# Performance work log

Hardware: AMD Instinct MI355X
Metric: run time of the kernel (lower is better)

Reference implementation:

```python
import jax, jax.numpy as jnp
import numpy as np

N = 200000
F_IN = 165
H = 128
E = 3200000


def gcn_conv(x, edge_index, W, b):
    # x: [N, Fin], edge_index: [2, E], W: [Fin, Fout], b: [Fout]
    n = x.shape[0]
    h = x @ W  # linear transform first (PyG GCNConv)
    # add self loops
    loops = jnp.arange(n, dtype=edge_index.dtype)
    src = jnp.concatenate([edge_index[0], loops])
    dst = jnp.concatenate([edge_index[1], loops])
    # symmetric normalization: deg computed on dst (in-degree incl. self loops)
    deg = jax.ops.segment_sum(jnp.ones_like(dst, dtype=h.dtype), dst, num_segments=n)
    dinv = jnp.where(deg > 0, jax.lax.rsqrt(deg), 0.0)
    norm = dinv[src] * dinv[dst]  # [E+N]
    msgs = h[src] * norm[:, None]  # gather + scale
    out = jax.ops.segment_sum(msgs, dst, num_segments=n)  # scatter-add
    return out + b


def setup_inputs() -> dict:
    key = jax.random.key(0)
    k = jax.random.split(key, 8)
    x = jax.random.normal(k[0], (N, F_IN), dtype=jnp.float32)
    edge_index = jax.random.randint(k[1], (2, E), 0, N, dtype=jnp.int64)
    s1 = 1.0 / np.sqrt(F_IN)
    s2 = 1.0 / np.sqrt(H)
    W1 = jax.random.uniform(k[2], (F_IN, H), jnp.float32, -s1, s1)
    b1 = jnp.zeros((H,), jnp.float32)
    W2 = jax.random.uniform(k[3], (H, H), jnp.float32, -s2, s2)
    b2 = jnp.zeros((H,), jnp.float32)
    Wl = jax.random.uniform(k[4], (H, 2), jnp.float32, -s2, s2)
    bl = jax.random.uniform(k[5], (2,), jnp.float32, -s2, s2)
    return {"x": x, "edge_index": edge_index, "W1": W1, "b1": b1,
            "W2": W2, "b2": b2, "Wl": Wl, "bl": bl}


def reference(x, edge_index, W1, b1, W2, b2, Wl, bl):
    h = gcn_conv(x, edge_index, W1, b1)
    h = jax.nn.relu(h)
    # dropout p=0.3 is identity in eval mode
    h = gcn_conv(h, edge_index, W2, b2)
    h = jax.nn.relu(h)
    return h @ Wl + bl  # [N, 2]
```

## Files before the change

### kernel.cpp

```cpp
#include <hip/hip_runtime.h>
#include <hip/hip_bf16.h>

#define FIN 165
#define HID 128
#define NPB 256
#define MAXNB 784
#define CAP 4608
#define EPB 2048

typedef __attribute__((ext_vector_type(8))) short short8;
typedef __attribute__((ext_vector_type(4))) float float4v;

__device__ inline unsigned bf16rne(float v) {
    unsigned u = __float_as_uint(v);
    return (u + 0x7fffu + ((u >> 16) & 1u)) >> 16;
}

__device__ inline void bf16split(float v, short& h, short& l) {
    unsigned u = __float_as_uint(v);
    unsigned r = u + 0x7fffu + ((u >> 16) & 1u);
    h = (short)(r >> 16);
    float hf = __uint_as_float(((unsigned)(unsigned short)h) << 16);
    float lf = v - hf;
    unsigned u2 = __float_as_uint(lf);
    unsigned r2 = u2 + 0x7fffu + ((u2 >> 16) & 1u);
    l = (short)(r2 >> 16);
}

__global__ __launch_bounds__(256) void bucket_scatter(const int* __restrict__ src,
                                                      const int* __restrict__ dst,
                                                      int* __restrict__ gcur,
                                                      unsigned* __restrict__ bucketed,
                                                      int E, int n, int NB) {
    __shared__ int hist[MAXNB];
    __shared__ int base[MAXNB];
    __shared__ int lcur[MAXNB];
    int tid = threadIdx.x;
    long e0 = (long)blockIdx.x * EPB;
    for (int b = tid; b < NB; b += 256) { hist[b] = 0; lcur[b] = 0; }
    __syncthreads();
    int sv[EPB / 256], dv[EPB / 256];
#pragma unroll
    for (int i = 0; i < EPB / 256; ++i) {
        long e = e0 + i * 256 + tid;
        sv[i] = (e < E) ? src[e] : -1;
        dv[i] = (e < E) ? dst[e] : -1;
        if ((unsigned)dv[i] < (unsigned)n && (unsigned)sv[i] < (unsigned)n)
            atomicAdd(&hist[dv[i] >> 8], 1);
    }
    __syncthreads();
    for (int b = tid; b < NB; b += 256) {
        int h = hist[b];
        base[b] = h ? atomicAdd(&gcur[b * 16], h) : 0;
    }
    __syncthreads();
#pragma unroll
    for (int i = 0; i < EPB / 256; ++i) {
        int d = dv[i], s = sv[i];
        if ((unsigned)d < (unsigned)n && (unsigned)s < (unsigned)n) {
            int bk = d >> 8;
            int idx = base[bk] + atomicAdd(&lcur[bk], 1);
            if ((unsigned)idx < (unsigned)CAP)
                bucketed[(size_t)bk * CAP + idx] =
                    (unsigned)s | ((unsigned)(d & 255) << 18);
        }
    }
}

__global__ __launch_bounds__(256) void bucket_scan(const int* __restrict__ gcur,
                                                   int* __restrict__ bb, int NB,
                                                   int* __restrict__ rowptr, int n) {
    __shared__ int part[256];
    int t = threadIdx.x;
    int v[4];
    int s = 0;
#pragma unroll
    for (int i = 0; i < 4; ++i) {
        int b = t * 4 + i;
        v[i] = (b < NB) ? gcur[b * 16] : 0;
        s += v[i];
    }
    part[t] = s;
    __syncthreads();
    for (int off = 1; off < 256; off <<= 1) {
        int x = (t >= off) ? part[t - off] : 0;
        __syncthreads();
        part[t] += x;
        __syncthreads();
    }
    int run = part[t] - s;
#pragma unroll
    for (int i = 0; i < 4; ++i) {
        int b = t * 4 + i;
        if (b < NB) bb[b] = run;
        run += v[i];
    }
    if (t == 255) { bb[NB] = run; rowptr[n] = run; }
}

__global__ __launch_bounds__(256) void build_csr(const unsigned* __restrict__ bucketed,
                                                 const int* __restrict__ bb,
                                                 float* __restrict__ dinv,
                                                 int* __restrict__ rowptr,
                                                 int* __restrict__ col, int n) {
    __shared__ int deg[NPB];
    __shared__ int scn[NPB];
    __shared__ int cur[NPB];
    int b = blockIdx.x, tid = threadIdx.x;
    int nb0 = b * NPB;
    int ebase = bb[b], cnt = bb[b + 1] - bb[b];
    deg[tid] = 0;
    __syncthreads();
    const unsigned* ep = bucketed + (size_t)b * CAP;
    for (int i = tid; i < cnt; i += 256) {
        unsigned v = ep[i];
        atomicAdd(&deg[(v >> 18) & 255], 1);
    }
    __syncthreads();
    int d = deg[tid];
    scn[tid] = d;
    __syncthreads();
    for (int off = 1; off < 256; off <<= 1) {
        int v = (tid >= off) ? scn[tid - off] : 0;
        __syncthreads();
        scn[tid] += v;
        __syncthreads();
    }
    int excl = scn[tid] - d;
    int node = nb0 + tid;
    if (node < n) {
        dinv[node] = rsqrtf((float)(d + 1));
        rowptr[node] = ebase + excl;
    }
    cur[tid] = excl;
    __syncthreads();
    for (int i = tid; i < cnt; i += 256) {
        unsigned v = ep[i];
        int p = atomicAdd(&cur[(v >> 18) & 255], 1);
        col[ebase + p] = (int)(v & 0x3FFFFu);
    }
}

__global__ __launch_bounds__(256) void wswz(const float* __restrict__ W,
                                            short8* __restrict__ out, int K, int k32) {
    int idx = blockIdx.x * 256 + threadIdx.x;
    int tot = k32 * 8 * 64;
    if (idx >= tot) return;
    int lane = idx & 63;
    int ct = (idx >> 6) & 7;
    int ks = idx >> 9;
    int col = ct * 16 + (lane & 15);
    int kb = ks * 32 + (lane >> 4) * 8;
    short8 hi, lo;
#pragma unroll
    for (int j = 0; j < 8; ++j) {
        int k = kb + j;
        float v = (k < K) ? W[k * HID + col] : 0.f;
        short h, l;
        bf16split(v, h, l);
        hi[j] = h; lo[j] = l;
    }
    out[idx] = hi;
    out[tot + idx] = lo;
}

__global__ __launch_bounds__(256) void gemm_mfma(const float* __restrict__ X,
                                                 const short8* __restrict__ Wsw,
                                                 const float* __restrict__ dinv,
                                                 unsigned* __restrict__ H2,
                                                 int n, int K, int kfull, int k32) {
    int wave = threadIdx.x >> 6, lane = threadIdx.x & 63;
    int r0 = blockIdx.x * 64 + wave * 16;
    int m = lane & 15, kph = lane >> 4;
    int row = r0 + m;
    const float* xrow = X + (size_t)row * K + kph * 8;
    const short8* Whi = Wsw;
    const short8* Wlo = Wsw + (size_t)k32 * 8 * 64;

    float4v acc[8];
#pragma unroll
    for (int ct = 0; ct < 8; ++ct) acc[ct] = (float4v){0.f, 0.f, 0.f, 0.f};

    for (int ks = 0; ks < kfull; ++ks) {
        float xv[8];
#pragma unroll
        for (int j = 0; j < 8; ++j) xv[j] = xrow[ks * 32 + j];
        short8 ah, al;
#pragma unroll
        for (int j = 0; j < 8; ++j) {
            short h, l; bf16split(xv[j], h, l);
            ah[j] = h; al[j] = l;
        }
#pragma unroll
        for (int ct = 0; ct < 8; ++ct) {
            short8 bh = Whi[(ks * 8 + ct) * 64 + lane];
            short8 bl = Wlo[(ks * 8 + ct) * 64 + lane];
            acc[ct] = __builtin_amdgcn_mfma_f32_16x16x32_bf16(ah, bh, acc[ct], 0, 0, 0);
            acc[ct] = __builtin_amdgcn_mfma_f32_16x16x32_bf16(al, bh, acc[ct], 0, 0, 0);
            acc[ct] = __builtin_amdgcn_mfma_f32_16x16x32_bf16(ah, bl, acc[ct], 0, 0, 0);
        }
    }
    if (kfull < k32) {
        int ks = kfull;
        int kb = ks * 32 + kph * 8;
        float xv[8];
#pragma unroll
        for (int j = 0; j < 8; ++j) xv[j] = (kb + j < K) ? xrow[ks * 32 + j] : 0.f;
        short8 ah, al;
#pragma unroll
        for (int j = 0; j < 8; ++j) {
            short h, l; bf16split(xv[j], h, l);
            ah[j] = h; al[j] = l;
        }
#pragma unroll
        for (int ct = 0; ct < 8; ++ct) {
            short8 bh = Whi[(ks * 8 + ct) * 64 + lane];
            short8 bl = Wlo[(ks * 8 + ct) * 64 + lane];
            acc[ct] = __builtin_amdgcn_mfma_f32_16x16x32_bf16(ah, bh, acc[ct], 0, 0, 0);
            acc[ct] = __builtin_amdgcn_mfma_f32_16x16x32_bf16(al, bh, acc[ct], 0, 0, 0);
            acc[ct] = __builtin_amdgcn_mfma_f32_16x16x32_bf16(ah, bl, acc[ct], 0, 0, 0);
        }
    }
    int ccol = lane & 15, crow = (lane >> 4) * 4;
    bool evenl = (ccol & 1) == 0;
#pragma unroll
    for (int r = 0; r < 4; ++r) {
        int gr = r0 + crow + r;
        float s = dinv[gr];
#pragma unroll
        for (int ct = 0; ct < 8; ++ct) {
            float v = acc[ct][r] * s;
            float p = __shfl_xor(v, 1);
            if (evenl) {
                unsigned u = bf16rne(v) | (bf16rne(p) << 16);
                H2[(size_t)gr * 64 + ct * 8 + (ccol >> 1)] = u;
            }
        }
    }
}

__device__ inline void bf2_unpack(unsigned u, float& f0, float& f1) {
    f0 = __uint_as_float(u << 16);
    f1 = __uint_as_float(u & 0xffff0000u);
}

__global__ __launch_bounds__(256) void agg_relu(const unsigned* __restrict__ HS2,
                                                const int* __restrict__ rowptr,
                                                const int* __restrict__ col,
                                                const float* __restrict__ dinv,
                                                const float* __restrict__ bias,
                                                float* __restrict__ Y, int n) {
    int lane = threadIdx.x & 63;
    int node = __builtin_amdgcn_readfirstlane(blockIdx.x * 4 + (threadIdx.x >> 6));
    if (node >= n) return;
    int start = __builtin_amdgcn_readfirstlane(rowptr[node]);
    int end   = __builtin_amdgcn_readfirstlane(rowptr[node + 1]);
    float2 acc;
    {
        float f0, f1;
        bf2_unpack(HS2[(size_t)node * 64 + lane], f0, f1);
        acc.x = f0; acc.y = f1;
    }
    int j = start;
    for (; j + 16 <= end; j += 16) {
        unsigned uv[16];
#pragma unroll
        for (int q = 0; q < 16; ++q) {
            int c = col[j + q];
            uv[q] = HS2[(size_t)c * 64 + lane];
        }
#pragma unroll
        for (int q = 0; q < 16; ++q) {
            float f0, f1; bf2_unpack(uv[q], f0, f1);
            acc.x += f0; acc.y += f1;
        }
    }
    while (j < end) {
        unsigned uv[8];
#pragma unroll
        for (int q = 0; q < 8; ++q) {
            int jq = j + q;
            int c = (jq < end) ? col[jq] : node;
            uv[q] = HS2[(size_t)c * 64 + lane];
        }
#pragma unroll
        for (int q = 0; q < 8; ++q) {
            unsigned u = (j + q < end) ? uv[q] : 0u;
            float f0, f1; bf2_unpack(u, f0, f1);
            acc.x += f0; acc.y += f1;
        }
        j += 8;
    }
    float s = dinv[node];
    float2 b = *(const float2*)&bias[2 * lane];
    float2 o;
    o.x = fmaxf(acc.x * s + b.x, 0.f);
    o.y = fmaxf(acc.y * s + b.y, 0.f);
    *(float2*)&Y[(long)node * HID + 2 * lane] = o;
}

__global__ __launch_bounds__(256) void agg_relu_head(const unsigned* __restrict__ HS2,
                                                     const int* __restrict__ rowptr,
                                                     const int* __restrict__ col,
                                                     const float* __restrict__ dinv,
                                                     const float* __restrict__ bias,
                                                     const float* __restrict__ Wl,
                                                     const float* __restrict__ bl,
                                                     float* __restrict__ out, int n) {
    int lane = threadIdx.x & 63;
    int node = __builtin_amdgcn_readfirstlane(blockIdx.x * 4 + (threadIdx.x >> 6));
    if (node >= n) return;
    int start = __builtin_amdgcn_readfirstlane(rowptr[node]);
    int end   = __builtin_amdgcn_readfirstlane(rowptr[node + 1]);
    float2 acc;
    {
        float f0, f1;
        bf2_unpack(HS2[(size_t)node * 64 + lane], f0, f1);
        acc.x = f0; acc.y = f1;
    }
    int j = start;
    for (; j + 16 <= end; j += 16) {
        unsigned uv[16];
#pragma unroll
        for (int q = 0; q < 16; ++q) {
            int c = col[j + q];
            uv[q] = HS2[(size_t)c * 64 + lane];
        }
#pragma unroll
        for (int q = 0; q < 16; ++q) {
            float f0, f1; bf2_unpack(uv[q], f0, f1);
            acc.x += f0; acc.y += f1;
        }
    }
    while (j < end) {
        unsigned uv[8];
#pragma unroll
        for (int q = 0; q < 8; ++q) {
            int jq = j + q;
            int c = (jq < end) ? col[jq] : node;
            uv[q] = HS2[(size_t)c * 64 + lane];
        }
#pragma unroll
        for (int q = 0; q < 8; ++q) {
            unsigned u = (j + q < end) ? uv[q] : 0u;
            float f0, f1; bf2_unpack(u, f0, f1);
            acc.x += f0; acc.y += f1;
        }
        j += 8;
    }
    float s = dinv[node];
    float2 b = *(const float2*)&bias[2 * lane];
    float vx = fmaxf(acc.x * s + b.x, 0.f);
    float vy = fmaxf(acc.y * s + b.y, 0.f);
    float4 wl = *(const float4*)&Wl[4 * lane];
    float a0 = vx * wl.x + vy * wl.z;
    float a1 = vx * wl.y + vy * wl.w;
#pragma unroll
    for (int off = 32; off > 0; off >>= 1) {
        a0 += __shfl_xor(a0, off);
        a1 += __shfl_xor(a1, off);
    }
    if (lane == 0) {
        out[node * 2 + 0] = a0 + bl[0];
        out[node * 2 + 1] = a1 + bl[1];
    }
}

extern "C" void kernel_launch(void* const* d_in, const int* in_sizes, int n_in,
                              void* d_out, int out_size, void* d_ws, size_t ws_size,
                              hipStream_t stream) {
    const float* x  = (const float*)d_in[0];
    const int*   ei = (const int*)d_in[1];
    const float* W1 = (const float*)d_in[2];
    const float* b1 = (const float*)d_in[3];
    const float* W2 = (const float*)d_in[4];
    const float* b2 = (const float*)d_in[5];
    const float* Wl = (const float*)d_in[6];
    const float* bl = (const float*)d_in[7];
    float* out = (float*)d_out;

    int n = in_sizes[0] / FIN;
    int E = in_sizes[1] / 2;
    int NB = (n + NPB - 1) / NPB;
    const int* srcp = ei;
    const int* dstp = ei + E;

    char* w = (char*)d_ws;
    auto alloc = [&](size_t bytes) {
        char* p = w;
        w += (bytes + 255) & ~(size_t)255;
        return (void*)p;
    };
    int*      gcur    = (int*)     alloc((size_t)NB * 16 * 4);
    int*      bb      = (int*)     alloc(((size_t)NB + 1) * 4);
    int*      rowptr  = (int*)     alloc(((size_t)n + 1) * 4);
    float*    dinv    = (float*)   alloc((size_t)n * 4);
    int*      colv    = (int*)     alloc((size_t)E * 4);
    unsigned* hbuf    = (unsigned*)alloc((size_t)n * 64 * 4);
    float*    ybuf    = (float*)   alloc((size_t)n * HID * 4);
    const int K32_1 = (FIN + 31) / 32;
    const int K32_2 = HID / 32;
    short8*   w1sw    = (short8*)  alloc((size_t)2 * K32_1 * 8 * 64 * 16);
    short8*   w2sw    = (short8*)  alloc((size_t)2 * K32_2 * 8 * 64 * 16);
    unsigned* bucketed = (unsigned*)ybuf;

    hipMemsetAsync(gcur, 0, (size_t)NB * 16 * 4, stream);

    wswz<<<(K32_1 * 8 * 64 + 255) / 256, 256, 0, stream>>>(W1, w1sw, FIN, K32_1);
    wswz<<<(K32_2 * 8 * 64 + 255) / 256, 256, 0, stream>>>(W2, w2sw, HID, K32_2);

    bucket_scatter<<<(E + EPB - 1) / EPB, 256, 0, stream>>>(srcp, dstp, gcur,
                                                            bucketed, E, n, NB);
    bucket_scan<<<1, 256, 0, stream>>>(gcur, bb, NB, rowptr, n);
    build_csr<<<NB, 256, 0, stream>>>(bucketed, bb, dinv, rowptr, colv, n);

    gemm_mfma<<<n / 64, 256, 0, stream>>>(x, w1sw, dinv, hbuf, n, FIN, FIN / 32, K32_1);
    agg_relu<<<(n + 3) / 4, 256, 0, stream>>>(hbuf, rowptr, colv, dinv, b1, ybuf, n);

    gemm_mfma<<<n / 64, 256, 0, stream>>>(ybuf, w2sw, dinv, hbuf, n, HID, HID / 32, K32_2);

    agg_relu_head<<<(n + 3) / 4, 256, 0, stream>>>(hbuf, rowptr, colv, dinv, b2,
                                                   Wl, bl, out, n);
}
```

Before: 701.5 us.

## Overlap edge bucketing with first GEMM and fold scan into last scatter block

Removes the dependency of the first GEMM on dinv by moving the source-side normalization into the aggregation kernels, which now gather dinv[c] per edge and apply it with an FMA. This lets the bucket-scatter blocks and the layer-1 GEMM blocks run in one fused launch. The separate scan kernel is replaced by a last-block-done pattern inside the scatter, and the two weight-swizzle launches are merged into one. The aggregation kernels gain an extra per-edge dinv load, and the GEMM output is no longer prescaled.

```diff
diff --git a/kernel.cpp b/kernel.cpp
--- a/kernel.cpp
+++ b/kernel.cpp
@@ -7,6 +7,8 @@
 #define MAXNB 784
 #define CAP 4608
 #define EPB 2048
+#define K32C1 6
+#define K32C2 4
 
 typedef __attribute__((ext_vector_type(8))) short short8;
 typedef __attribute__((ext_vector_type(4))) float float4v;
@@ -27,16 +29,142 @@
     l = (short)(r2 >> 16);
 }
 
-__global__ __launch_bounds__(256) void bucket_scatter(const int* __restrict__ src,
-                                                      const int* __restrict__ dst,
-                                                      int* __restrict__ gcur,
-                                                      unsigned* __restrict__ bucketed,
-                                                      int E, int n, int NB) {
+__device__ inline void bf2_unpack(unsigned u, float& f0, float& f1) {
+    f0 = __uint_as_float(u << 16);
+    f1 = __uint_as_float(u & 0xffff0000u);
+}
+
+__device__ inline void wswz_body(const float* W, short8* out, int K, int k32, int idx) {
+    int tot = k32 * 8 * 64;
+    if (idx >= tot) return;
+    int lane = idx & 63;
+    int ct = (idx >> 6) & 7;
+    int ks = idx >> 9;
+    int col = ct * 16 + (lane & 15);
+    int kb = ks * 32 + (lane >> 4) * 8;
+    short8 hi, lo;
+#pragma unroll
+    for (int j = 0; j < 8; ++j) {
+        int k = kb + j;
+        float v = (k < K) ? W[k * HID + col] : 0.f;
+        short h, l;
+        bf16split(v, h, l);
+        hi[j] = h; lo[j] = l;
+    }
+    out[idx] = hi;
+    out[tot + idx] = lo;
+}
+
+__global__ __launch_bounds__(256) void wswz_both(const float* __restrict__ W1p,
+                                                 short8* __restrict__ o1,
+                                                 const float* __restrict__ W2p,
+                                                 short8* __restrict__ o2) {
+    int bid = blockIdx.x;
+    if (bid < 12) wswz_body(W1p, o1, FIN, K32C1, bid * 256 + threadIdx.x);
+    else          wswz_body(W2p, o2, HID, K32C2, (bid - 12) * 256 + threadIdx.x);
+}
+
+__device__ void gemm_body(int bid, const float* __restrict__ X,
+                          const short8* __restrict__ Wsw,
+                          unsigned* __restrict__ H2, int K, int kfull, int k32) {
+    int wave = threadIdx.x >> 6, lane = threadIdx.x & 63;
+    int r0 = bid * 64 + wave * 16;
+    int m = lane & 15, kph = lane >> 4;
+    int row = r0 + m;
+    const float* xrow = X + (size_t)row * K + kph * 8;
+    const short8* Whi = Wsw;
+    const short8* Wlo = Wsw + (size_t)k32 * 8 * 64;
+
+    float4v acc[8];
+#pragma unroll
+    for (int ct = 0; ct < 8; ++ct) acc[ct] = (float4v){0.f, 0.f, 0.f, 0.f};
+
+    for (int ks = 0; ks < kfull; ++ks) {
+        float xv[8];
+#pragma unroll
+        for (int j = 0; j < 8; ++j) xv[j] = xrow[ks * 32 + j];
+        short8 ah, al;
+#pragma unroll
+        for (int j = 0; j < 8; ++j) {
+            short h, l; bf16split(xv[j], h, l);
+            ah[j] = h; al[j] = l;
+        }
+#pragma unroll
+        for (int ct = 0; ct < 8; ++ct) {
+            short8 bh = Whi[(ks * 8 + ct) * 64 + lane];
+            short8 bl = Wlo[(ks * 8 + ct) * 64 + lane];
+            acc[ct] = __builtin_amdgcn_mfma_f32_16x16x32_bf16(ah, bh, acc[ct], 0, 0, 0);
+            acc[ct] = __builtin_amdgcn_mfma_f32_16x16x32_bf16(al, bh, acc[ct], 0, 0, 0);
+            acc[ct] = __builtin_amdgcn_mfma_f32_16x16x32_bf16(ah, bl, acc[ct], 0, 0, 0);
+        }
+    }
+    if (kfull < k32) {
+        int ks = kfull;
+        int kb = ks * 32 + kph * 8;
+        float xv[8];
+#pragma unroll
+        for (int j = 0; j < 8; ++j) xv[j] = (kb + j < K) ? xrow[ks * 32 + j] : 0.f;
+        short8 ah, al;
+#pragma unroll
+        for (int j = 0; j < 8; ++j) {
+            short h, l; bf16split(xv[j], h, l);
+            ah[j] = h; al[j] = l;
+        }
+#pragma unroll
+        for (int ct = 0; ct < 8; ++ct) {
+            short8 bh = Whi[(ks * 8 + ct) * 64 + lane];
+            short8 bl = Wlo[(ks * 8 + ct) * 64 + lane];
+            acc[ct] = __builtin_amdgcn_mfma_f32_16x16x32_bf16(ah, bh, acc[ct], 0, 0, 0);
+            acc[ct] = __builtin_amdgcn_mfma_f32_16x16x32_bf16(al, bh, acc[ct], 0, 0, 0);
+            acc[ct] = __builtin_amdgcn_mfma_f32_16x16x32_bf16(ah, bl, acc[ct], 0, 0, 0);
+        }
+    }
+    int ccol = lane & 15, crow = (lane >> 4) * 4;
+    bool evenl = (ccol & 1) == 0;
+#pragma unroll
+    for (int r = 0; r < 4; ++r) {
+        int gr = r0 + crow + r;
+#pragma unroll
+        for (int ct = 0; ct < 8; ++ct) {
+            float v = acc[ct][r];
+            float p = __shfl_xor(v, 1);
+            if (evenl) {
+                unsigned u = bf16rne(v) | (bf16rne(p) << 16);
+                H2[(size_t)gr * 64 + ct * 8 + (ccol >> 1)] = u;
+            }
+        }
+    }
+}
+
+__global__ __launch_bounds__(256) void gemm_mfma(const float* __restrict__ X,
+                                                 const short8* __restrict__ Wsw,
+                                                 unsigned* __restrict__ H2,
+                                                 int K, int kfull, int k32) {
+    gemm_body(blockIdx.x, X, Wsw, H2, K, kfull, k32);
+}
+
+__global__ __launch_bounds__(256) void scatter_gemm(const int* __restrict__ src,
+                                                    const int* __restrict__ dst,
+                                                    int* __restrict__ gcur,
+                                                    unsigned* __restrict__ bucketed,
+                                                    int E, int n, int NB, int NSCAT,
+                                                    int* __restrict__ done,
+                                                    int* __restrict__ bb,
+                                                    int* __restrict__ rowptr,
+                                                    const float* __restrict__ X,
+                                                    const short8* __restrict__ Wsw,
+                                                    unsigned* __restrict__ H2,
+                                                    int K, int kfull, int k32) {
     __shared__ int hist[MAXNB];
     __shared__ int base[MAXNB];
     __shared__ int lcur[MAXNB];
+    int bid = blockIdx.x;
+    if (bid >= NSCAT) {
+        gemm_body(bid - NSCAT, X, Wsw, H2, K, kfull, k32);
+        return;
+    }
     int tid = threadIdx.x;
-    long e0 = (long)blockIdx.x * EPB;
+    long e0 = (long)bid * EPB;
     for (int b = tid; b < NB; b += 256) { hist[b] = 0; lcur[b] = 0; }
     __syncthreads();
     int sv[EPB / 256], dv[EPB / 256];
@@ -65,37 +193,38 @@
                     (unsigned)s | ((unsigned)(d & 255) << 18);
         }
     }
-}
-
-__global__ __launch_bounds__(256) void bucket_scan(const int* __restrict__ gcur,
-                                                   int* __restrict__ bb, int NB,
-                                                   int* __restrict__ rowptr, int n) {
+    __threadfence();
+    __syncthreads();
+    __shared__ int lastf;
+    if (tid == 0) lastf = (atomicAdd(done, 1) == NSCAT - 1) ? 1 : 0;
+    __syncthreads();
+    if (!lastf) return;
+    __threadfence();
     __shared__ int part[256];
-    int t = threadIdx.x;
     int v[4];
     int s = 0;
 #pragma unroll
     for (int i = 0; i < 4; ++i) {
-        int b = t * 4 + i;
-        v[i] = (b < NB) ? gcur[b * 16] : 0;
+        int b = tid * 4 + i;
+        v[i] = (b < NB) ? atomicAdd(&gcur[b * 16], 0) : 0;
         s += v[i];
     }
-    part[t] = s;
+    part[tid] = s;
     __syncthreads();
     for (int off = 1; off < 256; off <<= 1) {
-        int x = (t >= off) ? part[t - off] : 0;
+        int x = (tid >= off) ? part[tid - off] : 0;
         __syncthreads();
-        part[t] += x;
+        part[tid] += x;
         __syncthreads();
     }
-    int run = part[t] - s;
+    int run = part[tid] - s;
 #pragma unroll
     for (int i = 0; i < 4; ++i) {
-        int b = t * 4 + i;
+        int b = tid * 4 + i;
         if (b < NB) bb[b] = run;
         run += v[i];
     }
-    if (t == 255) { bb[NB] = run; rowptr[n] = run; }
+    if (tid == 255) { bb[NB] = run; rowptr[n] = run; }
 }
 
 __global__ __launch_bounds__(256) void build_csr(const unsigned* __restrict__ bucketed,
@@ -141,109 +270,6 @@
     }
 }
 
-__global__ __launch_bounds__(256) void wswz(const float* __restrict__ W,
-                                            short8* __restrict__ out, int K, int k32) {
-    int idx = blockIdx.x * 256 + threadIdx.x;
-    int tot = k32 * 8 * 64;
-    if (idx >= tot) return;
-    int lane = idx & 63;
-    int ct = (idx >> 6) & 7;
-    int ks = idx >> 9;
-    int col = ct * 16 + (lane & 15);
-    int kb = ks * 32 + (lane >> 4) * 8;
-    short8 hi, lo;
-#pragma unroll
-    for (int j = 0; j < 8; ++j) {
-        int k = kb + j;
-        float v = (k < K) ? W[k * HID + col] : 0.f;
-        short h, l;
-        bf16split(v, h, l);
-        hi[j] = h; lo[j] = l;
-    }
-    out[idx] = hi;
-    out[tot + idx] = lo;
-}
-
-__global__ __launch_bounds__(256) void gemm_mfma(const float* __restrict__ X,
-                                                 const short8* __restrict__ Wsw,
-                                                 const float* __restrict__ dinv,
-                                                 unsigned* __restrict__ H2,
-                                                 int n, int K, int kfull, int k32) {
-    int wave = threadIdx.x >> 6, lane = threadIdx.x & 63;
-    int r0 = blockIdx.x * 64 + wave * 16;
-    int m = lane & 15, kph = lane >> 4;
-    int row = r0 + m;
-    const float* xrow = X + (size_t)row * K + kph * 8;
-    const short8* Whi = Wsw;
-    const short8* Wlo = Wsw + (size_t)k32 * 8 * 64;
-
-    float4v acc[8];
-#pragma unroll
-    for (int ct = 0; ct < 8; ++ct) acc[ct] = (float4v){0.f, 0.f, 0.f, 0.f};
-
-    for (int ks = 0; ks < kfull; ++ks) {
-        float xv[8];
-#pragma unroll
-        for (int j = 0; j < 8; ++j) xv[j] = xrow[ks * 32 + j];
-        short8 ah, al;
-#pragma unroll
-        for (int j = 0; j < 8; ++j) {
-            short h, l; bf16split(xv[j], h, l);
-            ah[j] = h; al[j] = l;
-        }
-#pragma unroll
-        for (int ct = 0; ct < 8; ++ct) {
-            short8 bh = Whi[(ks * 8 + ct) * 64 + lane];
-            short8 bl = Wlo[(ks * 8 + ct) * 64 + lane];
-            acc[ct] = __builtin_amdgcn_mfma_f32_16x16x32_bf16(ah, bh, acc[ct], 0, 0, 0);
-            acc[ct] = __builtin_amdgcn_mfma_f32_16x16x32_bf16(al, bh, acc[ct], 0, 0, 0);
-            acc[ct] = __builtin_amdgcn_mfma_f32_16x16x32_bf16(ah, bl, acc[ct], 0, 0, 0);
-        }
-    }
-    if (kfull < k32) {
-        int ks = kfull;
-        int kb = ks * 32 + kph * 8;
-        float xv[8];
-#pragma unroll
-        for (int j = 0; j < 8; ++j) xv[j] = (kb + j < K) ? xrow[ks * 32 + j] : 0.f;
-        short8 ah, al;
-#pragma unroll
-        for (int j = 0; j < 8; ++j) {
-            short h, l; bf16split(xv[j], h, l);
-            ah[j] = h; al[j] = l;
-        }
-#pragma unroll
-        for (int ct = 0; ct < 8; ++ct) {
-            short8 bh = Whi[(ks * 8 + ct) * 64 + lane];
-            short8 bl = Wlo[(ks * 8 + ct) * 64 + lane];
-            acc[ct] = __builtin_amdgcn_mfma_f32_16x16x32_bf16(ah, bh, acc[ct], 0, 0, 0);
-            acc[ct] = __builtin_amdgcn_mfma_f32_16x16x32_bf16(al, bh, acc[ct], 0, 0, 0);
-            acc[ct] = __builtin_amdgcn_mfma_f32_16x16x32_bf16(ah, bl, acc[ct], 0, 0, 0);
-        }
-    }
-    int ccol = lane & 15, crow = (lane >> 4) * 4;
-    bool evenl = (ccol & 1) == 0;
-#pragma unroll
-    for (int r = 0; r < 4; ++r) {
-        int gr = r0 + crow + r;
-        float s = dinv[gr];
-#pragma unroll
-        for (int ct = 0; ct < 8; ++ct) {
-            float v = acc[ct][r] * s;
-            float p = __shfl_xor(v, 1);
-            if (evenl) {
-                unsigned u = bf16rne(v) | (bf16rne(p) << 16);
-                H2[(size_t)gr * 64 + ct * 8 + (ccol >> 1)] = u;
-            }
-        }
-    }
-}
-
-__device__ inline void bf2_unpack(unsigned u, float& f0, float& f1) {
-    f0 = __uint_as_float(u << 16);
-    f1 = __uint_as_float(u & 0xffff0000u);
-}
-
 __global__ __launch_bounds__(256) void agg_relu(const unsigned* __restrict__ HS2,
                                                 const int* __restrict__ rowptr,
                                                 const int* __restrict__ col,
@@ -255,47 +281,53 @@
     if (node >= n) return;
     int start = __builtin_amdgcn_readfirstlane(rowptr[node]);
     int end   = __builtin_amdgcn_readfirstlane(rowptr[node + 1]);
+    float dn = dinv[node];
     float2 acc;
     {
         float f0, f1;
         bf2_unpack(HS2[(size_t)node * 64 + lane], f0, f1);
-        acc.x = f0; acc.y = f1;
+        acc.x = f0 * dn; acc.y = f1 * dn;
     }
     int j = start;
     for (; j + 16 <= end; j += 16) {
         unsigned uv[16];
+        float dq[16];
 #pragma unroll
         for (int q = 0; q < 16; ++q) {
             int c = col[j + q];
+            dq[q] = dinv[c];
             uv[q] = HS2[(size_t)c * 64 + lane];
         }
 #pragma unroll
         for (int q = 0; q < 16; ++q) {
             float f0, f1; bf2_unpack(uv[q], f0, f1);
-            acc.x += f0; acc.y += f1;
+            acc.x = fmaf(f0, dq[q], acc.x);
+            acc.y = fmaf(f1, dq[q], acc.y);
         }
     }
     while (j < end) {
         unsigned uv[8];
+        float dq[8];
 #pragma unroll
         for (int q = 0; q < 8; ++q) {
             int jq = j + q;
             int c = (jq < end) ? col[jq] : node;
+            dq[q] = dinv[c];
             uv[q] = HS2[(size_t)c * 64 + lane];
         }
 #pragma unroll
         for (int q = 0; q < 8; ++q) {
             unsigned u = (j + q < end) ? uv[q] : 0u;
             float f0, f1; bf2_unpack(u, f0, f1);
-            acc.x += f0; acc.y += f1;
+            acc.x = fmaf(f0, dq[q], acc.x);
+            acc.y = fmaf(f1, dq[q], acc.y);
         }
         j += 8;
     }
-    float s = dinv[node];
     float2 b = *(const float2*)&bias[2 * lane];
     float2 o;
-    o.x = fmaxf(acc.x * s + b.x, 0.f);
-    o.y = fmaxf(acc.y * s + b.y, 0.f);
+    o.x = fmaxf(acc.x * dn + b.x, 0.f);
+    o.y = fmaxf(acc.y * dn + b.y, 0.f);
     *(float2*)&Y[(long)node * HID + 2 * lane] = o;
 }
 
@@ -312,46 +344,52 @@
     if (node >= n) return;
     int start = __builtin_amdgcn_readfirstlane(rowptr[node]);
     int end   = __builtin_amdgcn_readfirstlane(rowptr[node + 1]);
+    float dn = dinv[node];
     float2 acc;
     {
         float f0, f1;
         bf2_unpack(HS2[(size_t)node * 64 + lane], f0, f1);
-        acc.x = f0; acc.y = f1;
+        acc.x = f0 * dn; acc.y = f1 * dn;
     }
     int j = start;
     for (; j + 16 <= end; j += 16) {
         unsigned uv[16];
+        float dq[16];
 #pragma unroll
         for (int q = 0; q < 16; ++q) {
             int c = col[j + q];
+            dq[q] = dinv[c];
             uv[q] = HS2[(size_t)c * 64 + lane];
         }
 #pragma unroll
         for (int q = 0; q < 16; ++q) {
             float f0, f1; bf2_unpack(uv[q], f0, f1);
-            acc.x += f0; acc.y += f1;
+            acc.x = fmaf(f0, dq[q], acc.x);
+            acc.y = fmaf(f1, dq[q], acc.y);
         }
     }
     while (j < end) {
         unsigned uv[8];
+        float dq[8];
 #pragma unroll
         for (int q = 0; q < 8; ++q) {
             int jq = j + q;
             int c = (jq < end) ? col[jq] : node;
+            dq[q] = dinv[c];
             uv[q] = HS2[(size_t)c * 64 + lane];
         }
 #pragma unroll
         for (int q = 0; q < 8; ++q) {
             unsigned u = (j + q < end) ? uv[q] : 0u;
             float f0, f1; bf2_unpack(u, f0, f1);
-            acc.x += f0; acc.y += f1;
+            acc.x = fmaf(f0, dq[q], acc.x);
+            acc.y = fmaf(f1, dq[q], acc.y);
         }
         j += 8;
     }
-    float s = dinv[node];
     float2 b = *(const float2*)&bias[2 * lane];
-    float vx = fmaxf(acc.x * s + b.x, 0.f);
-    float vy = fmaxf(acc.y * s + b.y, 0.f);
+    float vx = fmaxf(acc.x * dn + b.x, 0.f);
+    float vy = fmaxf(acc.y * dn + b.y, 0.f);
     float4 wl = *(const float4*)&Wl[4 * lane];
     float a0 = vx * wl.x + vy * wl.z;
     float a1 = vx * wl.y + vy * wl.w;
@@ -361,8 +399,8 @@
         a1 += __shfl_xor(a1, off);
     }
     if (lane == 0) {
-        out[node * 2 + 0] = a0 + bl[0];
-        out[node * 2 + 1] = a1 + bl[1];
+        out[(long)node * 2 + 0] = a0 + bl[0];
+        out[(long)node * 2 + 1] = a1 + bl[1];
     }
 }
 
@@ -382,6 +420,7 @@
     int n = in_sizes[0] / FIN;
     int E = in_sizes[1] / 2;
     int NB = (n + NPB - 1) / NPB;
+    int NSCAT = (E + EPB - 1) / EPB;
     const int* srcp = ei;
     const int* dstp = ei + E;
 
@@ -391,33 +430,30 @@
         w += (bytes + 255) & ~(size_t)255;
         return (void*)p;
     };
-    int*      gcur    = (int*)     alloc((size_t)NB * 16 * 4);
+    int*      gcur    = (int*)     alloc(((size_t)NB * 16 + 16) * 4);
     int*      bb      = (int*)     alloc(((size_t)NB + 1) * 4);
     int*      rowptr  = (int*)     alloc(((size_t)n + 1) * 4);
     float*    dinv    = (float*)   alloc((size_t)n * 4);
     int*      colv    = (int*)     alloc((size_t)E * 4);
     unsigned* hbuf    = (unsigned*)alloc((size_t)n * 64 * 4);
     float*    ybuf    = (float*)   alloc((size_t)n * HID * 4);
-    const int K32_1 = (FIN + 31) / 32;
-    const int K32_2 = HID / 32;
-    short8*   w1sw    = (short8*)  alloc((size_t)2 * K32_1 * 8 * 64 * 16);
-    short8*   w2sw    = (short8*)  alloc((size_t)2 * K32_2 * 8 * 64 * 16);
+    short8*   w1sw    = (short8*)  alloc((size_t)2 * K32C1 * 8 * 64 * 16);
+    short8*   w2sw    = (short8*)  alloc((size_t)2 * K32C2 * 8 * 64 * 16);
     unsigned* bucketed = (unsigned*)ybuf;
-
-    hipMemsetAsync(gcur, 0, (size_t)NB * 16 * 4, stream);
-
-    wswz<<<(K32_1 * 8 * 64 + 255) / 256, 256, 0, stream>>>(W1, w1sw, FIN, K32_1);
-    wswz<<<(K32_2 * 8 * 64 + 255) / 256, 256, 0, stream>>>(W2, w2sw, HID, K32_2);
-
-    bucket_scatter<<<(E + EPB - 1) / EPB, 256, 0, stream>>>(srcp, dstp, gcur,
-                                                            bucketed, E, n, NB);
-    bucket_scan<<<1, 256, 0, stream>>>(gcur, bb, NB, rowptr, n);
+    int*      done     = gcur + (size_t)NB * 16;
+
+    hipMemsetAsync(gcur, 0, ((size_t)NB * 16 + 16) * 4, stream);
+
+    wswz_both<<<20, 256, 0, stream>>>(W1, w1sw, W2, w2sw);
+
+    scatter_gemm<<<NSCAT + n / 64, 256, 0, stream>>>(srcp, dstp, gcur, bucketed,
+                                                     E, n, NB, NSCAT, done, bb, rowptr,
+                                                     x, w1sw, hbuf, FIN, FIN / 32, K32C1);
     build_csr<<<NB, 256, 0, stream>>>(bucketed, bb, dinv, rowptr, colv, n);
 
-    gemm_mfma<<<n / 64, 256, 0, stream>>>(x, w1sw, dinv, hbuf, n, FIN, FIN / 32, K32_1);
     agg_relu<<<(n + 3) / 4, 256, 0, stream>>>(hbuf, rowptr, colv, dinv, b1, ybuf, n);
 
-    gemm_mfma<<<n / 64, 256, 0, stream>>>(ybuf, w2sw, dinv, hbuf, n, HID, HID / 32, K32_2);
+    gemm_mfma<<<n / 64, 256, 0, stream>>>(ybuf, w2sw, hbuf, HID, HID / 32, K32C2);
 
     agg_relu_head<<<(n + 3) / 4, 256, 0, stream>>>(hbuf, rowptr, colv, dinv, b2,
                                                    Wl, bl, out, n);
```

Result: slower. 1.048 ms (+49.5%).

## Merge CSR build with first GEMM and apply source dinv during aggregation

Applied to the files above, without the earlier changes.

Layer-1 GEMM no longer scales rows by dinv, so it can run in the same launch as the CSR build (block-index split), overlapping the two independent stages. The first aggregation now multiplies each gathered neighbour row by its own dinv[c], loaded per edge, to recover the normalization. The two weight-swizzle kernels are also merged into one launch. The cost is an extra per-edge dinv gather in agg_relu. Fusing the kernels may also change occupancy, since shared memory and registers are now sized for both bodies.

```diff
diff --git a/kernel.cpp b/kernel.cpp
--- a/kernel.cpp
+++ b/kernel.cpp
@@ -7,6 +7,8 @@
 #define MAXNB 784
 #define CAP 4608
 #define EPB 2048
+#define K32C1 6
+#define K32C2 4
 
 typedef __attribute__((ext_vector_type(8))) short short8;
 typedef __attribute__((ext_vector_type(4))) float float4v;
@@ -25,6 +27,41 @@
     unsigned u2 = __float_as_uint(lf);
     unsigned r2 = u2 + 0x7fffu + ((u2 >> 16) & 1u);
     l = (short)(r2 >> 16);
+}
+
+__device__ inline void bf2_unpack(unsigned u, float& f0, float& f1) {
+    f0 = __uint_as_float(u << 16);
+    f1 = __uint_as_float(u & 0xffff0000u);
+}
+
+__device__ inline void wswz_body(const float* W, short8* out, int K, int k32, int idx) {
+    int tot = k32 * 8 * 64;
+    if (idx >= tot) return;
+    int lane = idx & 63;
+    int ct = (idx >> 6) & 7;
+    int ks = idx >> 9;
+    int col = ct * 16 + (lane & 15);
+    int kb = ks * 32 + (lane >> 4) * 8;
+    short8 hi, lo;
+#pragma unroll
+    for (int j = 0; j < 8; ++j) {
+        int k = kb + j;
+        float v = (k < K) ? W[k * HID + col] : 0.f;
+        short h, l;
+        bf16split(v, h, l);
+        hi[j] = h; lo[j] = l;
+    }
+    out[idx] = hi;
+    out[tot + idx] = lo;
+}
+
+__global__ __launch_bounds__(256) void wswz_both(const float* __restrict__ W1p,
+                                                 short8* __restrict__ o1,
+                                                 const float* __restrict__ W2p,
+                                                 short8* __restrict__ o2) {
+    int bid = blockIdx.x;
+    if (bid < 12) wswz_body(W1p, o1, FIN, K32C1, bid * 256 + threadIdx.x);
+    else          wswz_body(W2p, o2, HID, K32C2, (bid - 12) * 256 + threadIdx.x);
 }
 
 __global__ __launch_bounds__(256) void bucket_scatter(const int* __restrict__ src,
@@ -98,79 +135,12 @@
     if (t == 255) { bb[NB] = run; rowptr[n] = run; }
 }
 
-__global__ __launch_bounds__(256) void build_csr(const unsigned* __restrict__ bucketed,
-                                                 const int* __restrict__ bb,
-                                                 float* __restrict__ dinv,
-                                                 int* __restrict__ rowptr,
-                                                 int* __restrict__ col, int n) {
-    __shared__ int deg[NPB];
-    __shared__ int scn[NPB];
-    __shared__ int cur[NPB];
-    int b = blockIdx.x, tid = threadIdx.x;
-    int nb0 = b * NPB;
-    int ebase = bb[b], cnt = bb[b + 1] - bb[b];
-    deg[tid] = 0;
-    __syncthreads();
-    const unsigned* ep = bucketed + (size_t)b * CAP;
-    for (int i = tid; i < cnt; i += 256) {
-        unsigned v = ep[i];
-        atomicAdd(&deg[(v >> 18) & 255], 1);
-    }
-    __syncthreads();
-    int d = deg[tid];
-    scn[tid] = d;
-    __syncthreads();
-    for (int off = 1; off < 256; off <<= 1) {
-        int v = (tid >= off) ? scn[tid - off] : 0;
-        __syncthreads();
-        scn[tid] += v;
-        __syncthreads();
-    }
-    int excl = scn[tid] - d;
-    int node = nb0 + tid;
-    if (node < n) {
-        dinv[node] = rsqrtf((float)(d + 1));
-        rowptr[node] = ebase + excl;
-    }
-    cur[tid] = excl;
-    __syncthreads();
-    for (int i = tid; i < cnt; i += 256) {
-        unsigned v = ep[i];
-        int p = atomicAdd(&cur[(v >> 18) & 255], 1);
-        col[ebase + p] = (int)(v & 0x3FFFFu);
-    }
-}
-
-__global__ __launch_bounds__(256) void wswz(const float* __restrict__ W,
-                                            short8* __restrict__ out, int K, int k32) {
-    int idx = blockIdx.x * 256 + threadIdx.x;
-    int tot = k32 * 8 * 64;
-    if (idx >= tot) return;
-    int lane = idx & 63;
-    int ct = (idx >> 6) & 7;
-    int ks = idx >> 9;
-    int col = ct * 16 + (lane & 15);
-    int kb = ks * 32 + (lane >> 4) * 8;
-    short8 hi, lo;
-#pragma unroll
-    for (int j = 0; j < 8; ++j) {
-        int k = kb + j;
-        float v = (k < K) ? W[k * HID + col] : 0.f;
-        short h, l;
-        bf16split(v, h, l);
-        hi[j] = h; lo[j] = l;
-    }
-    out[idx] = hi;
-    out[tot + idx] = lo;
-}
-
-__global__ __launch_bounds__(256) void gemm_mfma(const float* __restrict__ X,
-                                                 const short8* __restrict__ Wsw,
-                                                 const float* __restrict__ dinv,
-                                                 unsigned* __restrict__ H2,
-                                                 int n, int K, int kfull, int k32) {
+__device__ void gemm_body(int bid, const float* __restrict__ X,
+                          const short8* __restrict__ Wsw,
+                          const float* __restrict__ dinvp,
+                          unsigned* __restrict__ H2, int K, int kfull, int k32) {
     int wave = threadIdx.x >> 6, lane = threadIdx.x & 63;
-    int r0 = blockIdx.x * 64 + wave * 16;
+    int r0 = bid * 64 + wave * 16;
     int m = lane & 15, kph = lane >> 4;
     int row = r0 + m;
     const float* xrow = X + (size_t)row * K + kph * 8;
@@ -226,7 +196,7 @@
 #pragma unroll
     for (int r = 0; r < 4; ++r) {
         int gr = r0 + crow + r;
-        float s = dinv[gr];
+        float s = dinvp ? dinvp[gr] : 1.0f;
 #pragma unroll
         for (int ct = 0; ct < 8; ++ct) {
             float v = acc[ct][r] * s;
@@ -239,9 +209,69 @@
     }
 }
 
-__device__ inline void bf2_unpack(unsigned u, float& f0, float& f1) {
-    f0 = __uint_as_float(u << 16);
-    f1 = __uint_as_float(u & 0xffff0000u);
+__global__ __launch_bounds__(256) void gemm_mfma(const float* __restrict__ X,
+                                                 const short8* __restrict__ Wsw,
+                                                 const float* __restrict__ dinv,
+                                                 unsigned* __restrict__ H2,
+                                                 int K, int kfull, int k32) {
+    gemm_body(blockIdx.x, X, Wsw, dinv, H2, K, kfull, k32);
+}
+
+__device__ void build_csr_body(int b, const unsigned* __restrict__ bucketed,
+                               const int* __restrict__ bb,
+                               float* __restrict__ dinv,
+                               int* __restrict__ rowptr,
+                               int* __restrict__ col, int n) {
+    __shared__ int deg[NPB];
+    __shared__ int scn[NPB];
+    __shared__ int cur[NPB];
+    int tid = threadIdx.x;
+    int nb0 = b * NPB;
+    int ebase = bb[b], cnt = bb[b + 1] - bb[b];
+    deg[tid] = 0;
+    __syncthreads();
+    const unsigned* ep = bucketed + (size_t)b * CAP;
+    for (int i = tid; i < cnt; i += 256) {
+        unsigned v = ep[i];
+        atomicAdd(&deg[(v >> 18) & 255], 1);
+    }
+    __syncthreads();
+    int d = deg[tid];
+    scn[tid] = d;
+    __syncthreads();
+    for (int off = 1; off < 256; off <<= 1) {
+        int v = (tid >= off) ? scn[tid - off] : 0;
+        __syncthreads();
+        scn[tid] += v;
+        __syncthreads();
+    }
+    int excl = scn[tid] - d;
+    int node = nb0 + tid;
+    if (node < n) {
+        dinv[node] = rsqrtf((float)(d + 1));
+        rowptr[node] = ebase + excl;
+    }
+    cur[tid] = excl;
+    __syncthreads();
+    for (int i = tid; i < cnt; i += 256) {
+        unsigned v = ep[i];
+        int p = atomicAdd(&cur[(v >> 18) & 255], 1);
+        col[ebase + p] = (int)(v & 0x3FFFFu);
+    }
+}
+
+__global__ __launch_bounds__(256) void csr_gemm(const unsigned* __restrict__ bucketed,
+                                                const int* __restrict__ bb,
+                                                float* __restrict__ dinv,
+                                                int* __restrict__ rowptr,
+                                                int* __restrict__ col, int n, int NCSR,
+                                                const float* __restrict__ X,
+                                                const short8* __restrict__ Wsw,
+                                                unsigned* __restrict__ H2,
+                                                int K, int kfull, int k32) {
+    int bid = blockIdx.x;
+    if (bid < NCSR) build_csr_body(bid, bucketed, bb, dinv, rowptr, col, n);
+    else            gemm_body(bid - NCSR, X, Wsw, nullptr, H2, K, kfull, k32);
 }
 
 __global__ __launch_bounds__(256) void agg_relu(const unsigned* __restrict__ HS2,
@@ -255,47 +285,53 @@
     if (node >= n) return;
     int start = __builtin_amdgcn_readfirstlane(rowptr[node]);
     int end   = __builtin_amdgcn_readfirstlane(rowptr[node + 1]);
+    float dn = dinv[node];
     float2 acc;
     {
         float f0, f1;
         bf2_unpack(HS2[(size_t)node * 64 + lane], f0, f1);
-        acc.x = f0; acc.y = f1;
+        acc.x = f0 * dn; acc.y = f1 * dn;
     }
     int j = start;
     for (; j + 16 <= end; j += 16) {
         unsigned uv[16];
+        float dq[16];
 #pragma unroll
         for (int q = 0; q < 16; ++q) {
             int c = col[j + q];
+            dq[q] = dinv[c];
             uv[q] = HS2[(size_t)c * 64 + lane];
         }
 #pragma unroll
         for (int q = 0; q < 16; ++q) {
             float f0, f1; bf2_unpack(uv[q], f0, f1);
-            acc.x += f0; acc.y += f1;
+            acc.x = fmaf(f0, dq[q], acc.x);
+            acc.y = fmaf(f1, dq[q], acc.y);
         }
     }
     while (j < end) {
         unsigned uv[8];
+        float dq[8];
 #pragma unroll
         for (int q = 0; q < 8; ++q) {
             int jq = j + q;
             int c = (jq < end) ? col[jq] : node;
+            dq[q] = dinv[c];
             uv[q] = HS2[(size_t)c * 64 + lane];
         }
 #pragma unroll
         for (int q = 0; q < 8; ++q) {
             unsigned u = (j + q < end) ? uv[q] : 0u;
             float f0, f1; bf2_unpack(u, f0, f1);
-            acc.x += f0; acc.y += f1;
+            acc.x = fmaf(f0, dq[q], acc.x);
+            acc.y = fmaf(f1, dq[q], acc.y);
         }
         j += 8;
     }
-    float s = dinv[node];
     float2 b = *(const float2*)&bias[2 * lane];
     float2 o;
-    o.x = fmaxf(acc.x * s + b.x, 0.f);
-    o.y = fmaxf(acc.y * s + b.y, 0.f);
+    o.x = fmaxf(acc.x * dn + b.x, 0.f);
+    o.y = fmaxf(acc.y * dn + b.y, 0.f);
     *(float2*)&Y[(long)node * HID + 2 * lane] = o;
 }
 
@@ -361,8 +397,8 @@
         a1 += __shfl_xor(a1, off);
     }
     if (lane == 0) {
-        out[node * 2 + 0] = a0 + bl[0];
-        out[node * 2 + 1] = a1 + bl[1];
+        out[(long)node * 2 + 0] = a0 + bl[0];
+        out[(long)node * 2 + 1] = a1 + bl[1];
     }
 }
 
@@ -398,26 +434,24 @@
     int*      colv    = (int*)     alloc((size_t)E * 4);
     unsigned* hbuf    = (unsigned*)alloc((size_t)n * 64 * 4);
     float*    ybuf    = (float*)   alloc((size_t)n * HID * 4);
-    const int K32_1 = (FIN + 31) / 32;
-    const int K32_2 = HID / 32;
-    short8*   w1sw    = (short8*)  alloc((size_t)2 * K32_1 * 8 * 64 * 16);
-    short8*   w2sw    = (short8*)  alloc((size_t)2 * K32_2 * 8 * 64 * 16);
+    short8*   w1sw    = (short8*)  alloc((size_t)2 * K32C1 * 8 * 64 * 16);
+    short8*   w2sw    = (short8*)  alloc((size_t)2 * K32C2 * 8 * 64 * 16);
     unsigned* bucketed = (unsigned*)ybuf;
 
     hipMemsetAsync(gcur, 0, (size_t)NB * 16 * 4, stream);
 
-    wswz<<<(K32_1 * 8 * 64 + 255) / 256, 256, 0, stream>>>(W1, w1sw, FIN, K32_1);
-    wswz<<<(K32_2 * 8 * 64 + 255) / 256, 256, 0, stream>>>(W2, w2sw, HID, K32_2);
+    wswz_both<<<20, 256, 0, stream>>>(W1, w1sw, W2, w2sw);
 
     bucket_scatter<<<(E + EPB - 1) / EPB, 256, 0, stream>>>(srcp, dstp, gcur,
                                                             bucketed, E, n, NB);
     bucket_scan<<<1, 256, 0, stream>>>(gcur, bb, NB, rowptr, n);
-    build_csr<<<NB, 256, 0, stream>>>(bucketed, bb, dinv, rowptr, colv, n);
-
-    gemm_mfma<<<n / 64, 256, 0, stream>>>(x, w1sw, dinv, hbuf, n, FIN, FIN / 32, K32_1);
+
+    csr_gemm<<<NB + n / 64, 256, 0, stream>>>(bucketed, bb, dinv, rowptr, colv, n, NB,
+                                              x, w1sw, hbuf, FIN, FIN / 32, K32C1);
+
     agg_relu<<<(n + 3) / 4, 256, 0, stream>>>(hbuf, rowptr, colv, dinv, b1, ybuf, n);
 
-    gemm_mfma<<<n / 64, 256, 0, stream>>>(ybuf, w2sw, dinv, hbuf, n, HID, HID / 32, K32_2);
+    gemm_mfma<<<n / 64, 256, 0, stream>>>(ybuf, w2sw, dinv, hbuf, HID, HID / 32, K32C2);
 
     agg_relu_head<<<(n + 3) / 4, 256, 0, stream>>>(hbuf, rowptr, colv, dinv, b2,
                                                    Wl, bl, out, n);
```

After: 787.6 us. +12.3%, slower.

## Stage swizzled weights in LDS with persistent-grid GEMM tiles

Applied to the files above, without the earlier changes.

The GEMM kernels become persistent: a fixed grid loops over 64-row tiles. Each block first copies the swizzled bf16 weight fragments into LDS once, with the low part also staged for the second layer, instead of reloading them from global or cache for every tile. The two weight-swizzle launches are merged into one kernel, and output indexing in the head kernel is widened to 64-bit. The trade-off is lower occupancy from the large LDS footprint (about 48KB hi-only for layer 1, 64KB for layer 2), plus a fixed grid size that may not match the CU count.

```diff
diff --git a/kernel.cpp b/kernel.cpp
--- a/kernel.cpp
+++ b/kernel.cpp
@@ -7,6 +7,8 @@
 #define MAXNB 784
 #define CAP 4608
 #define EPB 2048
+#define K32C1 6
+#define K32C2 4
 
 typedef __attribute__((ext_vector_type(8))) short short8;
 typedef __attribute__((ext_vector_type(4))) float float4v;
@@ -25,6 +27,41 @@
     unsigned u2 = __float_as_uint(lf);
     unsigned r2 = u2 + 0x7fffu + ((u2 >> 16) & 1u);
     l = (short)(r2 >> 16);
+}
+
+__device__ inline void bf2_unpack(unsigned u, float& f0, float& f1) {
+    f0 = __uint_as_float(u << 16);
+    f1 = __uint_as_float(u & 0xffff0000u);
+}
+
+__device__ inline void wswz_body(const float* W, short8* out, int K, int k32, int idx) {
+    int tot = k32 * 8 * 64;
+    if (idx >= tot) return;
+    int lane = idx & 63;
+    int ct = (idx >> 6) & 7;
+    int ks = idx >> 9;
+    int col = ct * 16 + (lane & 15);
+    int kb = ks * 32 + (lane >> 4) * 8;
+    short8 hi, lo;
+#pragma unroll
+    for (int j = 0; j < 8; ++j) {
+        int k = kb + j;
+        float v = (k < K) ? W[k * HID + col] : 0.f;
+        short h, l;
+        bf16split(v, h, l);
+        hi[j] = h; lo[j] = l;
+    }
+    out[idx] = hi;
+    out[tot + idx] = lo;
+}
+
+__global__ __launch_bounds__(256) void wswz_both(const float* __restrict__ W1p,
+                                                 short8* __restrict__ o1,
+                                                 const float* __restrict__ W2p,
+                                                 short8* __restrict__ o2) {
+    int bid = blockIdx.x;
+    if (bid < 12) wswz_body(W1p, o1, FIN, K32C1, bid * 256 + threadIdx.x);
+    else          wswz_body(W2p, o2, HID, K32C2, (bid - 12) * 256 + threadIdx.x);
 }
 
 __global__ __launch_bounds__(256) void bucket_scatter(const int* __restrict__ src,
@@ -141,107 +178,93 @@
     }
 }
 
-__global__ __launch_bounds__(256) void wswz(const float* __restrict__ W,
-                                            short8* __restrict__ out, int K, int k32) {
-    int idx = blockIdx.x * 256 + threadIdx.x;
-    int tot = k32 * 8 * 64;
-    if (idx >= tot) return;
-    int lane = idx & 63;
-    int ct = (idx >> 6) & 7;
-    int ks = idx >> 9;
-    int col = ct * 16 + (lane & 15);
-    int kb = ks * 32 + (lane >> 4) * 8;
-    short8 hi, lo;
-#pragma unroll
-    for (int j = 0; j < 8; ++j) {
-        int k = kb + j;
-        float v = (k < K) ? W[k * HID + col] : 0.f;
-        short h, l;
-        bf16split(v, h, l);
-        hi[j] = h; lo[j] = l;
-    }
-    out[idx] = hi;
-    out[tot + idx] = lo;
-}
-
-__global__ __launch_bounds__(256) void gemm_mfma(const float* __restrict__ X,
-                                                 const short8* __restrict__ Wsw,
-                                                 const float* __restrict__ dinv,
-                                                 unsigned* __restrict__ H2,
-                                                 int n, int K, int kfull, int k32) {
-    int wave = threadIdx.x >> 6, lane = threadIdx.x & 63;
-    int r0 = blockIdx.x * 64 + wave * 16;
+template <int K32, bool LO_IN_LDS>
+__global__ __launch_bounds__(256) void gemm_lds(const float* __restrict__ X,
+                                                const short8* __restrict__ Wsw,
+                                                const float* __restrict__ dinv,
+                                                unsigned* __restrict__ H2,
+                                                int K, int kfull, int ntiles) {
+    __shared__ short8 sh_hi[K32 * 8 * 64];
+    __shared__ short8 sh_lo[LO_IN_LDS ? K32 * 8 * 64 : 1];
+    const int tot = K32 * 8 * 64;
+    int tid = threadIdx.x;
+    for (int i = tid; i < tot; i += 256) sh_hi[i] = Wsw[i];
+    if (LO_IN_LDS)
+        for (int i = tid; i < tot; i += 256) sh_lo[i] = Wsw[tot + i];
+    __syncthreads();
+    const short8* wlo_g = Wsw + tot;
+
+    int wave = tid >> 6, lane = tid & 63;
     int m = lane & 15, kph = lane >> 4;
-    int row = r0 + m;
-    const float* xrow = X + (size_t)row * K + kph * 8;
-    const short8* Whi = Wsw;
-    const short8* Wlo = Wsw + (size_t)k32 * 8 * 64;
-
-    float4v acc[8];
-#pragma unroll
-    for (int ct = 0; ct < 8; ++ct) acc[ct] = (float4v){0.f, 0.f, 0.f, 0.f};
-
-    for (int ks = 0; ks < kfull; ++ks) {
-        float xv[8];
-#pragma unroll
-        for (int j = 0; j < 8; ++j) xv[j] = xrow[ks * 32 + j];
-        short8 ah, al;
-#pragma unroll
-        for (int j = 0; j < 8; ++j) {
-            short h, l; bf16split(xv[j], h, l);
-            ah[j] = h; al[j] = l;
-        }
-#pragma unroll
-        for (int ct = 0; ct < 8; ++ct) {
-            short8 bh = Whi[(ks * 8 + ct) * 64 + lane];
-            short8 bl = Wlo[(ks * 8 + ct) * 64 + lane];
-            acc[ct] = __builtin_amdgcn_mfma_f32_16x16x32_bf16(ah, bh, acc[ct], 0, 0, 0);
-            acc[ct] = __builtin_amdgcn_mfma_f32_16x16x32_bf16(al, bh, acc[ct], 0, 0, 0);
-            acc[ct] = __builtin_amdgcn_mfma_f32_16x16x32_bf16(ah, bl, acc[ct], 0, 0, 0);
-        }
-    }
-    if (kfull < k32) {
-        int ks = kfull;
-        int kb = ks * 32 + kph * 8;
-        float xv[8];
-#pragma unroll
-        for (int j = 0; j < 8; ++j) xv[j] = (kb + j < K) ? xrow[ks * 32 + j] : 0.f;
-        short8 ah, al;
-#pragma unroll
-        for (int j = 0; j < 8; ++j) {
-            short h, l; bf16split(xv[j], h, l);
-            ah[j] = h; al[j] = l;
-        }
-#pragma unroll
-        for (int ct = 0; ct < 8; ++ct) {
-            short8 bh = Whi[(ks * 8 + ct) * 64 + lane];
-            short8 bl = Wlo[(ks * 8 + ct) * 64 + lane];
-            acc[ct] = __builtin_amdgcn_mfma_f32_16x16x32_bf16(ah, bh, acc[ct], 0, 0, 0);
-            acc[ct] = __builtin_amdgcn_mfma_f32_16x16x32_bf16(al, bh, acc[ct], 0, 0, 0);
-            acc[ct] = __builtin_amdgcn_mfma_f32_16x16x32_bf16(ah, bl, acc[ct], 0, 0, 0);
-        }
-    }
-    int ccol = lane & 15, crow = (lane >> 4) * 4;
-    bool evenl = (ccol & 1) == 0;
-#pragma unroll
-    for (int r = 0; r < 4; ++r) {
-        int gr = r0 + crow + r;
-        float s = dinv[gr];
-#pragma unroll
-        for (int ct = 0; ct < 8; ++ct) {
-            float v = acc[ct][r] * s;
-            float p = __shfl_xor(v, 1);
-            if (evenl) {
-                unsigned u = bf16rne(v) | (bf16rne(p) << 16);
-                H2[(size_t)gr * 64 + ct * 8 + (ccol >> 1)] = u;
+
+    for (int t = blockIdx.x; t < ntiles; t += gridDim.x) {
+        int r0 = t * 64 + wave * 16;
+        int row = r0 + m;
+        const float* xrow = X + (size_t)row * K + kph * 8;
+
+        float4v acc[8];
+#pragma unroll
+        for (int ct = 0; ct < 8; ++ct) acc[ct] = (float4v){0.f, 0.f, 0.f, 0.f};
+
+        for (int ks = 0; ks < kfull; ++ks) {
+            float xv[8];
+#pragma unroll
+            for (int j = 0; j < 8; ++j) xv[j] = xrow[ks * 32 + j];
+            short8 ah, al;
+#pragma unroll
+            for (int j = 0; j < 8; ++j) {
+                short h, l; bf16split(xv[j], h, l);
+                ah[j] = h; al[j] = l;
             }
-        }
-    }
-}
-
-__device__ inline void bf2_unpack(unsigned u, float& f0, float& f1) {
-    f0 = __uint_as_float(u << 16);
-    f1 = __uint_as_float(u & 0xffff0000u);
+#pragma unroll
+            for (int ct = 0; ct < 8; ++ct) {
+                short8 bh = sh_hi[(ks * 8 + ct) * 64 + lane];
+                short8 bl = LO_IN_LDS ? sh_lo[(ks * 8 + ct) * 64 + lane]
+                                      : wlo_g[(ks * 8 + ct) * 64 + lane];
+                acc[ct] = __builtin_amdgcn_mfma_f32_16x16x32_bf16(ah, bh, acc[ct], 0, 0, 0);
+                acc[ct] = __builtin_amdgcn_mfma_f32_16x16x32_bf16(al, bh, acc[ct], 0, 0, 0);
+                acc[ct] = __builtin_amdgcn_mfma_f32_16x16x32_bf16(ah, bl, acc[ct], 0, 0, 0);
+            }
+        }
+        if (kfull < K32) {
+            int ks = kfull;
+            int kb = ks * 32 + kph * 8;
+            float xv[8];
+#pragma unroll
+            for (int j = 0; j < 8; ++j) xv[j] = (kb + j < K) ? xrow[ks * 32 + j] : 0.f;
+            short8 ah, al;
+#pragma unroll
+            for (int j = 0; j < 8; ++j) {
+                short h, l; bf16split(xv[j], h, l);
+                ah[j] = h; al[j] = l;
+            }
+#pragma unroll
+            for (int ct = 0; ct < 8; ++ct) {
+                short8 bh = sh_hi[(ks * 8 + ct) * 64 + lane];
+                short8 bl = LO_IN_LDS ? sh_lo[(ks * 8 + ct) * 64 + lane]
+                                      : wlo_g[(ks * 8 + ct) * 64 + lane];
+                acc[ct] = __builtin_amdgcn_mfma_f32_16x16x32_bf16(ah, bh, acc[ct], 0, 0, 0);
+                acc[ct] = __builtin_amdgcn_mfma_f32_16x16x32_bf16(al, bh, acc[ct], 0, 0, 0);
+                acc[ct] = __builtin_amdgcn_mfma_f32_16x16x32_bf16(ah, bl, acc[ct], 0, 0, 0);
+            }
+        }
+        int ccol = lane & 15, crow = (lane >> 4) * 4;
+        bool evenl = (ccol & 1) == 0;
+#pragma unroll
+        for (int r = 0; r < 4; ++r) {
+            int gr = r0 + crow + r;
+            float s = dinv[gr];
+#pragma unroll
+            for (int ct = 0; ct < 8; ++ct) {
+                float v = acc[ct][r] * s;
+                float p = __shfl_xor(v, 1);
+                if (evenl) {
+                    unsigned u = bf16rne(v) | (bf16rne(p) << 16);
+                    H2[(size_t)gr * 64 + ct * 8 + (ccol >> 1)] = u;
+                }
+            }
+        }
+    }
 }
 
 __global__ __launch_bounds__(256) void agg_relu(const unsigned* __restrict__ HS2,
@@ -361,8 +384,8 @@
         a1 += __shfl_xor(a1, off);
     }
     if (lane == 0) {
-        out[node * 2 + 0] = a0 + bl[0];
-        out[node * 2 + 1] = a1 + bl[1];
+        out[(long)node * 2 + 0] = a0 + bl[0];
+        out[(long)node * 2 + 1] = a1 + bl[1];
     }
 }
 
@@ -382,6 +405,7 @@
     int n = in_sizes[0] / FIN;
     int E = in_sizes[1] / 2;
     int NB = (n + NPB - 1) / NPB;
+    int ntiles = n / 64;
     const int* srcp = ei;
     const int* dstp = ei + E;
 
@@ -398,26 +422,25 @@
     int*      colv    = (int*)     alloc((size_t)E * 4);
     unsigned* hbuf    = (unsigned*)alloc((size_t)n * 64 * 4);
     float*    ybuf    = (float*)   alloc((size_t)n * HID * 4);
-    const int K32_1 = (FIN + 31) / 32;
-    const int K32_2 = HID / 32;
-    short8*   w1sw    = (short8*)  alloc((size_t)2 * K32_1 * 8 * 64 * 16);
-    short8*   w2sw    = (short8*)  alloc((size_t)2 * K32_2 * 8 * 64 * 16);
+    short8*   w1sw    = (short8*)  alloc((size_t)2 * K32C1 * 8 * 64 * 16);
+    short8*   w2sw    = (short8*)  alloc((size_t)2 * K32C2 * 8 * 64 * 16);
     unsigned* bucketed = (unsigned*)ybuf;
 
     hipMemsetAsync(gcur, 0, (size_t)NB * 16 * 4, stream);
 
-    wswz<<<(K32_1 * 8 * 64 + 255) / 256, 256, 0, stream>>>(W1, w1sw, FIN, K32_1);
-    wswz<<<(K32_2 * 8 * 64 + 255) / 256, 256, 0, stream>>>(W2, w2sw, HID, K32_2);
+    wswz_both<<<20, 256, 0, stream>>>(W1, w1sw, W2, w2sw);
 
     bucket_scatter<<<(E + EPB - 1) / EPB, 256, 0, stream>>>(srcp, dstp, gcur,
                                                             bucketed, E, n, NB);
     bucket_scan<<<1, 256, 0, stream>>>(gcur, bb, NB, rowptr, n);
     build_csr<<<NB, 256, 0, stream>>>(bucketed, bb, dinv, rowptr, colv, n);
 
-    gemm_mfma<<<n / 64, 256, 0, stream>>>(x, w1sw, dinv, hbuf, n, FIN, FIN / 32, K32_1);
+    gemm_lds<K32C1, false><<<768, 256, 0, stream>>>(x, w1sw, dinv, hbuf,
+                                                    FIN, FIN / 32, ntiles);
     agg_relu<<<(n + 3) / 4, 256, 0, stream>>>(hbuf, rowptr, colv, dinv, b1, ybuf, n);
 
-    gemm_mfma<<<n / 64, 256, 0, stream>>>(ybuf, w2sw, dinv, hbuf, n, HID, HID / 32, K32_2);
+    gemm_lds<K32C2, true><<<512, 256, 0, stream>>>(ybuf, w2sw, dinv, hbuf,
+                                                   HID, HID / 32, ntiles);
 
     agg_relu_head<<<(n + 3) / 4, 256, 0, stream>>>(hbuf, rowptr, colv, dinv, b2,
                                                    Wl, bl, out, n);
```

New measurement: 674.4 us (median of 2 runs). 1.04x faster.
